# Kernel tuning notes

Measured on AMD Instinct MI355X. Metric: run time of the kernel, lower is better.

Reference implementation:

```python
import jax, jax.numpy as jnp
import numpy as np

B, P, J, MOT, K, NB, WN, H = 64, 12273, 80, 94, 64, 20, 17, 128
W_POSE = 1.0

def euler_to_rotmat(a):
    # a: [..., 3] radians, R = Rz @ Ry @ Rx
    sx, sy, sz = jnp.sin(a[..., 0]), jnp.sin(a[..., 1]), jnp.sin(a[..., 2])
    cx, cy, cz = jnp.cos(a[..., 0]), jnp.cos(a[..., 1]), jnp.cos(a[..., 2])
    r00 = cz * cy; r01 = cz * sy * sx - sz * cx; r02 = cz * sy * cx + sz * sx
    r10 = sz * cy; r11 = sz * sy * sx + cz * cx; r12 = sz * sy * cx - cz * sx
    r20 = -sy;     r21 = cy * sx;                r22 = cy * cx
    return jnp.stack([jnp.stack([r00, r01, r02], -1),
                      jnp.stack([r10, r11, r12], -1),
                      jnp.stack([r20, r21, r22], -1)], -2)

def setup_inputs() -> dict:
    key = jax.random.key(0)
    ks = jax.random.split(key, 20)
    f32 = jnp.float32
    return {
        'in_pc_batch': jax.random.normal(ks[0], (B, P, 3), f32),
        't_nor': jax.random.normal(ks[1], (B, P, 3), f32),
        'rest_verts': jax.random.normal(ks[2], (P, 3), f32),
        'skin_weights': jax.random.uniform(ks[3], (P, J), f32),
        'mul_weight_list': jax.random.normal(ks[4], (J, MOT), f32),
        'query': jax.random.normal(ks[5], (B, J, 3), f32),
        'cloth_pose_std': jax.random.uniform(ks[6], (3,), f32),
        'cloth_pose_mean': jax.random.normal(ks[7], (3,), f32),
        'cloth_trans_std': jax.random.uniform(ks[8], (3,), f32),
        'cloth_trans_mean': jax.random.normal(ks[9], (3,), f32),
        'W1': jax.random.normal(ks[10], (3 + K, H), f32) * 0.1,
        'b1': jnp.zeros((H,), f32),
        'W2': jax.random.normal(ks[11], (H, 6), f32) * 0.1,
        'b2': jnp.zeros((6,), f32),
        'tmtemp': jax.random.normal(ks[12], (B, MOT, K), f32),
        'Wd': jax.random.normal(ks[13], (MOT * K, NB * WN), f32) * 0.02,
        'bd': jnp.zeros((NB * WN,), f32),
        'DPSD': jax.random.normal(ks[14], (NB, WN, P, 3), f32) * 0.1,
        'ssdr_res_std': jax.random.uniform(ks[15], (3,), f32),
        'ssdr_res_mean': jax.random.normal(ks[16], (3,), f32),
    }

def reference(in_pc_batch, t_nor, rest_verts, skin_weights, mul_weight_list,
              query, cloth_pose_std, cloth_pose_mean, cloth_trans_std,
              cloth_trans_mean, W1, b1, W2, b2, tmtemp, Wd, bd, DPSD,
              ssdr_res_std, ssdr_res_mean):
    # per-joint field input: [B, J, K]
    field_input = jnp.einsum('bjk,lj->blk', tmtemp, jax.nn.relu(mul_weight_list))
    # FieldNet: per-joint MLP on concat(query, field_input) -> [B, J, 6]
    h = jnp.concatenate([query, field_input], axis=-1)
    pred_rt = jax.nn.relu(h @ W1 + b1) @ W2 + b2
    pred_pose = pred_rt[..., 0:3] * cloth_pose_std + cloth_pose_mean
    pred_trans = (query + pred_rt[..., 3:6]) * cloth_trans_std + cloth_trans_mean
    # detailsnet + fused 20-basis accumulation: [B, P, 3]
    nbat = tmtemp.shape[0]
    detailkey = (tmtemp.reshape(nbat, -1) @ Wd + bd).reshape(nbat, NB, WN)
    detail_res = jnp.einsum('bnw,nwpx->bpx', detailkey, DPSD)
    detail_res = detail_res * ssdr_res_std + ssdr_res_mean
    # SSDR LBS skinning with Euler-angle rotations (degrees -> radians)
    R = euler_to_rotmat(jnp.deg2rad(pred_pose))            # [B, J, 3, 3]
    skinned = (jnp.einsum('pj,bjxy,py->bpx', skin_weights, R, rest_verts)
               + jnp.einsum('pj,bjx->bpx', skin_weights, pred_trans))
    out_pc = skinned + detail_res                          # [B, P, 3]
    loss_pose_l1 = jnp.mean(jnp.abs(in_pc_batch[:, :, 0:3] - out_pc))
    loss = loss_pose_l1 * W_POSE + 1e-4 * jnp.mean(DPSD ** 2)
    return loss[None], out_pc
```

## Files before the change

kernel.cpp:

```cpp
#include <hip/hip_runtime.h>

#define B_   64
#define P_   12273
#define J_   80
#define MOT_ 94
#define K_   64
#define H_   128
#define Q_   340
#define NE_  36819
#define MK_  6016
#define PW_  12288
#define STG_ 2356416

typedef float v4f  __attribute__((ext_vector_type(4)));
typedef float v8f  __attribute__((ext_vector_type(8)));
typedef float v16f __attribute__((ext_vector_type(16)));
#define AS4 __attribute__((address_space(4)))

__device__ __forceinline__ const AS4 float* unif(const float* p){
  return (const AS4 float*)(unsigned long long)p;
}
__device__ __forceinline__ const AS4 v4f* univ4(const float* p){
  return (const AS4 v4f*)(unsigned long long)p;
}
__device__ __forceinline__ const AS4 v16f* univ16(const float* p){
  return (const AS4 v16f*)(unsigned long long)p;
}

__global__ __launch_bounds__(256) void k_prep(
    const float* __restrict__ query, const float* __restrict__ mwl,
    const float* __restrict__ tm,    const float* __restrict__ W1,
    const float* __restrict__ b1,    const float* __restrict__ W2,
    const float* __restrict__ b2,    const float* __restrict__ cps,
    const float* __restrict__ cpm,   const float* __restrict__ cts,
    const float* __restrict__ ctm,   const float* __restrict__ skin,
    float* __restrict__ G,           float* __restrict__ tm_t,
    float* __restrict__ w_t,         float* __restrict__ lacc)
{
  __shared__ float smem[80 * 65];
  int blk = blockIdx.x;
  int t = threadIdx.x;
  if (blk < 1280){
    int lane = t & 63;
    int wid = __builtin_amdgcn_readfirstlane(t >> 6);
    int bj = blk * 4 + wid;
    int b = bj / J_, l = bj - b * J_;
    float* hs = smem + wid * 80;
    float acc = 0.f;
    const AS4 float* mp = unif(mwl + l * MOT_);
    const float* tp = tm + (size_t)b * MK_ + lane;
    float tbuf[4];
    #pragma unroll
    for (int s = 0; s < 4; s++) tbuf[s] = tp[s * K_];
    #pragma unroll 4
    for (int j = 0; j < MOT_; j++){
      float tv = tbuf[j & 3];
      if (j + 4 < MOT_) tbuf[j & 3] = tp[(j + 4) * K_];
      float w = mp[j]; w = w > 0.f ? w : 0.f;
      acc = fmaf(w, tv, acc);
    }
    hs[3 + lane] = acc;
    if (lane < 3) hs[lane] = query[(size_t)bj * 3 + lane];
    __syncthreads();
    float a1 = b1[lane], a2 = b1[lane + 64];
    float wa[4], wb[4];
    #pragma unroll
    for (int s = 0; s < 4; s++){
      wa[s] = W1[s * H_ + lane];
      wb[s] = W1[s * H_ + 64 + lane];
    }
    #pragma unroll 4
    for (int i = 0; i < 67; i++){
      float hv = hs[i];
      float va = wa[i & 3], vb = wb[i & 3];
      if (i + 4 < 67){
        wa[i & 3] = W1[(i + 4) * H_ + lane];
        wb[i & 3] = W1[(i + 4) * H_ + 64 + lane];
      }
      a1 = fmaf(hv, va, a1);
      a2 = fmaf(hv, vb, a2);
    }
    a1 = a1 > 0.f ? a1 : 0.f;
    a2 = a2 > 0.f ? a2 : 0.f;
    const AS4 float* b2c = unif(b2);
    float rt[6];
    #pragma unroll
    for (int o = 0; o < 6; o++){
      float po = fmaf(a1, W2[lane * 6 + o], a2 * W2[(lane + 64) * 6 + o]);
      #pragma unroll
      for (int off = 32; off; off >>= 1) po += __shfl_xor(po, off);
      rt[o] = po + b2c[o];
    }
    const float D2R = 0.017453292519943295f;
    float ax = fmaf(rt[0], cps[0], cpm[0]) * D2R;
    float ay = fmaf(rt[1], cps[1], cpm[1]) * D2R;
    float az = fmaf(rt[2], cps[2], cpm[2]) * D2R;
    float tx = fmaf(hs[0] + rt[3], cts[0], ctm[0]);
    float ty = fmaf(hs[1] + rt[4], cts[1], ctm[1]);
    float tz = fmaf(hs[2] + rt[5], cts[2], ctm[2]);
    float sx, cx, sy, cy, sz, cz;
    sincosf(ax, &sx, &cx); sincosf(ay, &sy, &cy); sincosf(az, &sz, &cz);
    if (lane == 0){
      float4 r0 = make_float4(cz*cy, cz*sy*sx - sz*cx, cz*sy*cx + sz*sx, tx);
      float4 r1 = make_float4(sz*cy, sz*sy*sx + cz*cx, sz*sy*cx - cz*sx, ty);
      float4 r2 = make_float4(-sy,   cy*sx,            cy*cx,            tz);
      float4* g = (float4*)(G + (size_t)bj * 12);
      g[0] = r0; g[1] = r1; g[2] = r2;
    }
  } else if (blk < 1374){
    int m0 = (blk - 1280) * 64;
    int ml = t & 63, g = t >> 6;
    #pragma unroll
    for (int r = 0; r < 16; r++){
      int b = g * 16 + r;
      smem[ml * 65 + b] = tm[(size_t)b * MK_ + m0 + ml];
    }
    __syncthreads();
    int bl = t & 63;
    #pragma unroll
    for (int r = 0; r < 16; r++){
      int m = g * 16 + r;
      tm_t[(size_t)(m0 + m) * 64 + bl] = smem[m * 65 + bl];
    }
  } else if (blk < 1566){
    int p0 = (blk - 1374) * 64;
    #pragma unroll
    for (int k = 0; k < 20; k++){
      int idx = k * 256 + t;
      int pl = idx / 80, j = idx - pl * 80;
      int p = p0 + pl;
      smem[j * 65 + pl] = (p < P_) ? skin[(size_t)p * J_ + j] : 0.f;
    }
    __syncthreads();
    #pragma unroll
    for (int k = 0; k < 20; k++){
      int idx = k * 256 + t;
      int j = idx >> 6, pl = idx & 63;
      w_t[(size_t)j * PW_ + p0 + pl] = smem[j * 65 + pl];
    }
  } else {
    if (t < 2) lacc[t] = 0.f;
  }
}

__global__ __launch_bounds__(256) void k_dkey(
    const float* __restrict__ tm_t, const float* __restrict__ Wd,
    float* __restrict__ part)
{
  int t = threadIdx.x;
  int lane = t & 63;
  int wid = __builtin_amdgcn_readfirstlane(t >> 6);
  int qt = blockIdx.x;
  int q = qt * 64 + lane;
  bool vq = q < Q_;
  int m0 = blockIdx.y * 64;
  const AS4 v16f* tr = univ16(tm_t);
  float acc[16];
  #pragma unroll
  for (int i = 0; i < 16; i++) acc[i] = 0.f;
  float wbuf[4];
  #pragma unroll
  for (int i = 0; i < 4; i++)
    wbuf[i] = vq ? Wd[(size_t)(m0 + i) * Q_ + q] : 0.f;
  v16f tb0 = tr[(size_t)(m0 + 0) * 4 + wid];
  v16f tb1 = tr[(size_t)(m0 + 1) * 4 + wid];
  #pragma unroll 4
  for (int mm = 0; mm < 60; mm++){
    float wd = wbuf[mm & 3];
    wbuf[mm & 3] = vq ? Wd[(size_t)(m0 + mm + 4) * Q_ + q] : 0.f;
    v16f tv = tb0; tb0 = tb1;
    tb1 = tr[(size_t)(m0 + mm + 2) * 4 + wid];
    #pragma unroll
    for (int i = 0; i < 16; i++) acc[i] = fmaf(tv[i], wd, acc[i]);
  }
  #pragma unroll
  for (int mm = 60; mm < 64; mm++){
    float wd = wbuf[mm & 3];
    v16f tv = tb0; tb0 = tb1;
    if (mm < 62) tb1 = tr[(size_t)(m0 + mm + 2) * 4 + wid];
    #pragma unroll
    for (int i = 0; i < 16; i++) acc[i] = fmaf(tv[i], wd, acc[i]);
  }
  float* pb = part + ((size_t)blockIdx.y * 6 + qt) * 4096 + (size_t)(wid * 16) * 64;
  #pragma unroll
  for (int i = 0; i < 16; i++) pb[i * 64 + lane] = acc[i];
}

__global__ __launch_bounds__(256) void k_dkred(
    const float* __restrict__ part, const float* __restrict__ bd,
    float* __restrict__ dk_t, int S)
{
  int t = threadIdx.x;
  int jj = blockIdx.x * 32 + (t >> 3);
  int dl = t & 7;
  int b = jj / Q_, q = jj - b * Q_;
  int qt = q >> 6, ql = q & 63;
  const float* pp = part + (size_t)qt * 4096 + b * 64 + ql;
  float s = 0.f;
  for (int d = dl; d < S; d += 8) s += pp[(size_t)d * 6 * 4096];
  s += __shfl_xor(s, 1); s += __shfl_xor(s, 2); s += __shfl_xor(s, 4);
  if (dl == 0) dk_t[q * 64 + b] = bd[q] + s;
}

__device__ __forceinline__ void dk_consume(const AS4 v16f* dkv, int qa, int wid,
                                           const float* dc, float* acc,
                                           float& sq, bool doSq)
{
  v16f r0 = dkv[(qa + 0) * 4 + wid];
  v16f r1 = dkv[(qa + 1) * 4 + wid];
  v16f r2 = dkv[(qa + 2) * 4 + wid];
  v16f r3 = dkv[(qa + 3) * 4 + wid];
  v16f r4 = dkv[(qa + 4) * 4 + wid];
  if (doSq){
    #pragma unroll
    for (int i = 0; i < 5; i++) sq = fmaf(dc[i], dc[i], sq);
  }
  #pragma unroll
  for (int i = 0; i < 16; i++){
    acc[i] = fmaf(r0[i], dc[0], acc[i]);
    acc[i] = fmaf(r1[i], dc[1], acc[i]);
    acc[i] = fmaf(r2[i], dc[2], acc[i]);
    acc[i] = fmaf(r3[i], dc[3], acc[i]);
    acc[i] = fmaf(r4[i], dc[4], acc[i]);
  }
}

__global__ __launch_bounds__(256) void k_detail(
    const float* __restrict__ DPSD, const float* __restrict__ dk_t,
    float* __restrict__ stg, float* __restrict__ out,
    float* __restrict__ lacc, int qn)
{
  int t = threadIdx.x;
  int lane = t & 63;
  int wid = __builtin_amdgcn_readfirstlane(t >> 6);
  int b0 = wid * 16;
  int e = blockIdx.x * 64 + lane;
  bool ve = e < NE_;
  int q0 = blockIdx.y * qn;
  const AS4 v16f* dkv = univ16(dk_t);
  const float* Dp = DPSD + (ve ? e : 0);
  float acc[16];
  #pragma unroll
  for (int i = 0; i < 16; i++) acc[i] = 0.f;
  float sq = 0.f;
  bool doSq = (wid == 0);
  int ng = qn / 5;
  float buf[4][5];
  #pragma unroll
  for (int s = 0; s < 4; s++){
    #pragma unroll
    for (int i = 0; i < 5; i++)
      buf[s][i] = Dp[(size_t)(q0 + s * 5 + i) * NE_];
  }
  for (int g = 0; g < ng; g += 4){
    #pragma unroll
    for (int s = 0; s < 4; s++){
      int gg = g + s;
      if (gg < ng){
        dk_consume(dkv, q0 + gg * 5, wid, buf[s], acc, sq, doSq);
        int gp = gg + 4;
        if (gp < ng){
          #pragma unroll
          for (int i = 0; i < 5; i++)
            buf[s][i] = Dp[(size_t)(q0 + gp * 5 + i) * NE_];
        }
      }
    }
  }
  if (ve){
    bool toOut = (blockIdx.y + 1 == gridDim.y);
    float* dst = toOut ? (out + 1 + e) : (stg + (size_t)blockIdx.y * STG_ + e);
    #pragma unroll
    for (int i = 0; i < 16; i++)
      dst[(size_t)(b0 + i) * NE_] = acc[i];
  }
  if (doSq){
    if (!ve) sq = 0.f;
    #pragma unroll
    for (int off = 32; off; off >>= 1) sq += __shfl_xor(sq, off);
    if (lane == 0) atomicAdd(&lacc[1], sq);
  }
}

__global__ __launch_bounds__(256) void k_skin(
    const float* __restrict__ G, const float* __restrict__ w_t,
    const float* __restrict__ rest, const float* __restrict__ in_pc,
    const float* __restrict__ stg, const float* __restrict__ rstd,
    const float* __restrict__ rmean,
    float* __restrict__ out, float* __restrict__ lacc, int nst)
{
  __shared__ float gs[7680];
  __shared__ float red[4];
  int t = threadIdx.x;
  int lane = t & 63;
  int wid = __builtin_amdgcn_readfirstlane(t >> 6);
  {
    const float4* Gv = (const float4*)(G + (size_t)blockIdx.y * 7680);
    float4* gv = (float4*)gs;
    #pragma unroll
    for (int it = 0; it < 8; it++){
      int idx = it * 256 + t;
      if (idx < 1920) gv[idx] = Gv[idx];
    }
  }
  __syncthreads();
  int p  = blockIdx.x * 64 + lane;
  int bA = blockIdx.y * 8 + wid * 2;
  const float4* gsA = (const float4*)(gs + (wid * 2) * 960);
  const float4* gsB = gsA + 240;
  float accA[12], accB[12];
  #pragma unroll
  for (int c = 0; c < 12; c++){ accA[c] = 0.f; accB[c] = 0.f; }
  const float* wp = w_t + p;
  float wbuf[8];
  #pragma unroll
  for (int s = 0; s < 8; s++) wbuf[s] = wp[(size_t)s * PW_];
  #pragma unroll 8
  for (int j = 0; j < J_; j++){
    float w = wbuf[j & 7];
    if (j + 8 < J_) wbuf[j & 7] = wp[(size_t)(j + 8) * PW_];
    float4 a0 = gsA[j * 3], a1 = gsA[j * 3 + 1], a2 = gsA[j * 3 + 2];
    float4 c0 = gsB[j * 3], c1 = gsB[j * 3 + 1], c2 = gsB[j * 3 + 2];
    accA[0]  = fmaf(w, a0.x, accA[0]);  accA[1]  = fmaf(w, a0.y, accA[1]);
    accA[2]  = fmaf(w, a0.z, accA[2]);  accA[3]  = fmaf(w, a0.w, accA[3]);
    accA[4]  = fmaf(w, a1.x, accA[4]);  accA[5]  = fmaf(w, a1.y, accA[5]);
    accA[6]  = fmaf(w, a1.z, accA[6]);  accA[7]  = fmaf(w, a1.w, accA[7]);
    accA[8]  = fmaf(w, a2.x, accA[8]);  accA[9]  = fmaf(w, a2.y, accA[9]);
    accA[10] = fmaf(w, a2.z, accA[10]); accA[11] = fmaf(w, a2.w, accA[11]);
    accB[0]  = fmaf(w, c0.x, accB[0]);  accB[1]  = fmaf(w, c0.y, accB[1]);
    accB[2]  = fmaf(w, c0.z, accB[2]);  accB[3]  = fmaf(w, c0.w, accB[3]);
    accB[4]  = fmaf(w, c1.x, accB[4]);  accB[5]  = fmaf(w, c1.y, accB[5]);
    accB[6]  = fmaf(w, c1.z, accB[6]);  accB[7]  = fmaf(w, c1.w, accB[7]);
    accB[8]  = fmaf(w, c2.x, accB[8]);  accB[9]  = fmaf(w, c2.y, accB[9]);
    accB[10] = fmaf(w, c2.z, accB[10]); accB[11] = fmaf(w, c2.w, accB[11]);
  }
  bool vp = p < P_;
  float vx = 0.f, vy = 0.f, vz = 0.f;
  if (vp){ vx = rest[p * 3]; vy = rest[p * 3 + 1]; vz = rest[p * 3 + 2]; }
  float srs[3], srm[3];
  #pragma unroll
  for (int x = 0; x < 3; x++){ srs[x] = rstd[x]; srm[x] = rmean[x]; }
  float lsum = 0.f;
  if (vp){
    size_t baseA = ((size_t)bA * P_ + p) * 3;
    size_t baseB = baseA + (size_t)P_ * 3;
    #pragma unroll
    for (int x = 0; x < 3; x++){
      float det = out[1 + baseA + x];
      for (int s = 0; s < nst; s++) det += stg[(size_t)s * STG_ + baseA + x];
      float v = fmaf(accA[x*4+0], vx, fmaf(accA[x*4+1], vy, fmaf(accA[x*4+2], vz, accA[x*4+3])));
      v += fmaf(det, srs[x], srm[x]);
      lsum += fabsf(in_pc[baseA + x] - v);
      out[1 + baseA + x] = v;
    }
    #pragma unroll
    for (int x = 0; x < 3; x++){
      float det = out[1 + baseB + x];
      for (int s = 0; s < nst; s++) det += stg[(size_t)s * STG_ + baseB + x];
      float v = fmaf(accB[x*4+0], vx, fmaf(accB[x*4+1], vy, fmaf(accB[x*4+2], vz, accB[x*4+3])));
      v += fmaf(det, srs[x], srm[x]);
      lsum += fabsf(in_pc[baseB + x] - v);
      out[1 + baseB + x] = v;
    }
  }
  #pragma unroll
  for (int off = 32; off; off >>= 1) lsum += __shfl_xor(lsum, off);
  if (lane == 0) red[wid] = lsum;
  __syncthreads();
  if (t == 0) atomicAdd(&lacc[0], red[0] + red[1] + red[2] + red[3]);
}

__global__ void k_finalize(const float* __restrict__ lacc, float* __restrict__ out){
  if (threadIdx.x == 0 && blockIdx.x == 0){
    float loss = lacc[0] * (1.f / 2356416.f) + 1e-4f * (lacc[1] * (1.f / 12518460.f));
    out[0] = loss;
  }
}

extern "C" void kernel_launch(void* const* d_in, const int* in_sizes, int n_in,
                              void* d_out, int out_size, void* d_ws, size_t ws_size,
                              hipStream_t stream){
  const float* in_pc = (const float*)d_in[0];
  const float* rest  = (const float*)d_in[2];
  const float* skin  = (const float*)d_in[3];
  const float* mwl   = (const float*)d_in[4];
  const float* query = (const float*)d_in[5];
  const float* cps   = (const float*)d_in[6];
  const float* cpm   = (const float*)d_in[7];
  const float* cts   = (const float*)d_in[8];
  const float* ctm   = (const float*)d_in[9];
  const float* W1    = (const float*)d_in[10];
  const float* b1    = (const float*)d_in[11];
  const float* W2    = (const float*)d_in[12];
  const float* b2    = (const float*)d_in[13];
  const float* tm    = (const float*)d_in[14];
  const float* Wd    = (const float*)d_in[15];
  const float* bd    = (const float*)d_in[16];
  const float* DPSD  = (const float*)d_in[17];
  const float* rstd  = (const float*)d_in[18];
  const float* rmean = (const float*)d_in[19];
  float* out = (float*)d_out;

  float* ws   = (float*)d_ws;
  float* G    = ws;
  float* dk_t = G + 61440;
  float* lacc = dk_t + 21760;
  float* tm_t = lacc + 64;
  float* w_t  = tm_t + 385024;
  float* un   = w_t + 983040;

  size_t have = ws_size / 4;
  int nqh = (have >= (size_t)(1451328 + 2356416)) ? 2 : 1;
  int qn = Q_ / nqh;

  k_prep    <<<1567, 256, 0, stream>>>(query, mwl, tm, W1, b1, W2, b2,
                                       cps, cpm, cts, ctm, skin,
                                       G, tm_t, w_t, lacc);
  k_dkey    <<<dim3(6, 94), 256, 0, stream>>>(tm_t, Wd, un);
  k_dkred   <<<680, 256, 0, stream>>>(un, bd, dk_t, 94);
  k_detail  <<<dim3(576, nqh), 256, 0, stream>>>(DPSD, dk_t, un, out, lacc, qn);
  k_skin    <<<dim3(192, 8), 256, 0, stream>>>(G, w_t, rest, in_pc, un, rstd, rmean,
                                               out, lacc, nqh - 1);
  k_finalize<<<1, 64, 0, stream>>>(lacc, out);
}
```

Measured before the change: 310.3 us.

## Process two element columns per thread in detail and skin kernels

k_detail now has each thread handle two DPSD columns (e1, e2), so every detail-key vector loaded from constant memory feeds twice as many FMAs. The grid is halved and the software pipeline is restructured into a two-group double buffer. k_skin likewise processes two points per thread, drops the LDS staging of G in favour of scalar/constant loads, and halves its grid. This doubles register pressure and reduces occupancy and block count, which may expose memory latency in these bandwidth-heavy kernels.

Result: faster. 296.9 us (-4.3%).

```diff
diff --git a/kernel.cpp b/kernel.cpp
--- a/kernel.cpp
+++ b/kernel.cpp
@@ -202,26 +202,23 @@
   if (dl == 0) dk_t[q * 64 + b] = bd[q] + s;
 }
 
-__device__ __forceinline__ void dk_consume(const AS4 v16f* dkv, int qa, int wid,
-                                           const float* dc, float* acc,
-                                           float& sq, bool doSq)
-{
-  v16f r0 = dkv[(qa + 0) * 4 + wid];
-  v16f r1 = dkv[(qa + 1) * 4 + wid];
-  v16f r2 = dkv[(qa + 2) * 4 + wid];
-  v16f r3 = dkv[(qa + 3) * 4 + wid];
-  v16f r4 = dkv[(qa + 4) * 4 + wid];
-  if (doSq){
-    #pragma unroll
-    for (int i = 0; i < 5; i++) sq = fmaf(dc[i], dc[i], sq);
-  }
-  #pragma unroll
-  for (int i = 0; i < 16; i++){
-    acc[i] = fmaf(r0[i], dc[0], acc[i]);
-    acc[i] = fmaf(r1[i], dc[1], acc[i]);
-    acc[i] = fmaf(r2[i], dc[2], acc[i]);
-    acc[i] = fmaf(r3[i], dc[3], acc[i]);
-    acc[i] = fmaf(r4[i], dc[4], acc[i]);
+__device__ __forceinline__ void dk_consume2(const AS4 v16f* dkv, int qa, int wid,
+                                            const float* dc1, const float* dc2,
+                                            float* acc1, float* acc2,
+                                            float& sq1, float& sq2, bool doSq)
+{
+  #pragma unroll
+  for (int qi = 0; qi < 5; qi++){
+    v16f r = dkv[(size_t)(qa + qi) * 4 + wid];
+    if (doSq){
+      sq1 = fmaf(dc1[qi], dc1[qi], sq1);
+      sq2 = fmaf(dc2[qi], dc2[qi], sq2);
+    }
+    #pragma unroll
+    for (int i = 0; i < 16; i++){
+      acc1[i] = fmaf(r[i], dc1[qi], acc1[i]);
+      acc2[i] = fmaf(r[i], dc2[qi], acc2[i]);
+    }
   }
 }
 
@@ -234,48 +231,71 @@
   int lane = t & 63;
   int wid = __builtin_amdgcn_readfirstlane(t >> 6);
   int b0 = wid * 16;
-  int e = blockIdx.x * 64 + lane;
-  bool ve = e < NE_;
+  int e1 = blockIdx.x * 128 + lane;
+  int e2 = e1 + 64;
+  bool ve1 = e1 < NE_;
+  bool ve2 = e2 < NE_;
   int q0 = blockIdx.y * qn;
   const AS4 v16f* dkv = univ16(dk_t);
-  const float* Dp = DPSD + (ve ? e : 0);
-  float acc[16];
-  #pragma unroll
-  for (int i = 0; i < 16; i++) acc[i] = 0.f;
-  float sq = 0.f;
+  const float* Dp1 = DPSD + (ve1 ? e1 : 0);
+  const float* Dp2 = DPSD + (ve2 ? e2 : 0);
+  float acc1[16], acc2[16];
+  #pragma unroll
+  for (int i = 0; i < 16; i++){ acc1[i] = 0.f; acc2[i] = 0.f; }
+  float sq1 = 0.f, sq2 = 0.f;
   bool doSq = (wid == 0);
   int ng = qn / 5;
-  float buf[4][5];
-  #pragma unroll
-  for (int s = 0; s < 4; s++){
-    #pragma unroll
-    for (int i = 0; i < 5; i++)
-      buf[s][i] = Dp[(size_t)(q0 + s * 5 + i) * NE_];
-  }
-  for (int g = 0; g < ng; g += 4){
-    #pragma unroll
-    for (int s = 0; s < 4; s++){
-      int gg = g + s;
-      if (gg < ng){
-        dk_consume(dkv, q0 + gg * 5, wid, buf[s], acc, sq, doSq);
-        int gp = gg + 4;
-        if (gp < ng){
-          #pragma unroll
-          for (int i = 0; i < 5; i++)
-            buf[s][i] = Dp[(size_t)(q0 + gp * 5 + i) * NE_];
-        }
-      }
-    }
-  }
-  if (ve){
-    bool toOut = (blockIdx.y + 1 == gridDim.y);
-    float* dst = toOut ? (out + 1 + e) : (stg + (size_t)blockIdx.y * STG_ + e);
-    #pragma unroll
-    for (int i = 0; i < 16; i++)
-      dst[(size_t)(b0 + i) * NE_] = acc[i];
+  float da1[5], da2[5], db1[5], db2[5];
+  #pragma unroll
+  for (int i = 0; i < 5; i++){
+    da1[i] = Dp1[(size_t)(q0 + i) * NE_];
+    da2[i] = Dp2[(size_t)(q0 + i) * NE_];
+  }
+  #pragma unroll
+  for (int i = 0; i < 5; i++){
+    db1[i] = Dp1[(size_t)(q0 + 5 + i) * NE_];
+    db2[i] = Dp2[(size_t)(q0 + 5 + i) * NE_];
+  }
+  for (int g = 0; g + 2 < ng; g += 2){
+    int qa = q0 + g * 5;
+    float ta1[5], ta2[5], tb1[5], tb2[5];
+    #pragma unroll
+    for (int i = 0; i < 5; i++){
+      ta1[i] = Dp1[(size_t)(qa + 10 + i) * NE_];
+      ta2[i] = Dp2[(size_t)(qa + 10 + i) * NE_];
+    }
+    #pragma unroll
+    for (int i = 0; i < 5; i++){
+      tb1[i] = Dp1[(size_t)(qa + 15 + i) * NE_];
+      tb2[i] = Dp2[(size_t)(qa + 15 + i) * NE_];
+    }
+    dk_consume2(dkv, qa,     wid, da1, da2, acc1, acc2, sq1, sq2, doSq);
+    dk_consume2(dkv, qa + 5, wid, db1, db2, acc1, acc2, sq1, sq2, doSq);
+    #pragma unroll
+    for (int i = 0; i < 5; i++){ da1[i] = ta1[i]; da2[i] = ta2[i]; }
+    #pragma unroll
+    for (int i = 0; i < 5; i++){ db1[i] = tb1[i]; db2[i] = tb2[i]; }
+  }
+  dk_consume2(dkv, q0 + (ng - 2) * 5, wid, da1, da2, acc1, acc2, sq1, sq2, doSq);
+  dk_consume2(dkv, q0 + (ng - 1) * 5, wid, db1, db2, acc1, acc2, sq1, sq2, doSq);
+  bool toOut = (blockIdx.y + 1 == gridDim.y);
+  {
+    float* dst = (toOut ? (out + 1) : (stg + (size_t)blockIdx.y * STG_));
+    if (ve1){
+      #pragma unroll
+      for (int i = 0; i < 16; i++)
+        dst[(size_t)(b0 + i) * NE_ + e1] = acc1[i];
+    }
+    if (ve2){
+      #pragma unroll
+      for (int i = 0; i < 16; i++)
+        dst[(size_t)(b0 + i) * NE_ + e2] = acc2[i];
+    }
   }
   if (doSq){
-    if (!ve) sq = 0.f;
+    if (!ve1) sq1 = 0.f;
+    if (!ve2) sq2 = 0.f;
+    float sq = sq1 + sq2;
     #pragma unroll
     for (int off = 32; off; off >>= 1) sq += __shfl_xor(sq, off);
     if (lane == 0) atomicAdd(&lacc[1], sq);
@@ -289,66 +309,56 @@
     const float* __restrict__ rmean,
     float* __restrict__ out, float* __restrict__ lacc, int nst)
 {
-  __shared__ float gs[7680];
-  __shared__ float red[4];
   int t = threadIdx.x;
   int lane = t & 63;
   int wid = __builtin_amdgcn_readfirstlane(t >> 6);
-  {
-    const float4* Gv = (const float4*)(G + (size_t)blockIdx.y * 7680);
-    float4* gv = (float4*)gs;
-    #pragma unroll
-    for (int it = 0; it < 8; it++){
-      int idx = it * 256 + t;
-      if (idx < 1920) gv[idx] = Gv[idx];
-    }
-  }
-  __syncthreads();
-  int p  = blockIdx.x * 64 + lane;
+  int p1 = blockIdx.x * 128 + lane;
+  int p2 = p1 + 64;
   int bA = blockIdx.y * 8 + wid * 2;
-  const float4* gsA = (const float4*)(gs + (wid * 2) * 960);
-  const float4* gsB = gsA + 240;
-  float accA[12], accB[12];
-  #pragma unroll
-  for (int c = 0; c < 12; c++){ accA[c] = 0.f; accB[c] = 0.f; }
-  const float* wp = w_t + p;
-  float wbuf[8];
-  #pragma unroll
-  for (int s = 0; s < 8; s++) wbuf[s] = wp[(size_t)s * PW_];
-  #pragma unroll 8
+  const AS4 v4f* gA = univ4(G + (size_t)bA * J_ * 12);
+  const AS4 v4f* gB = univ4(G + ((size_t)bA + 1) * J_ * 12);
+  float aA1[12], aA2[12], aB1[12], aB2[12];
+  #pragma unroll
+  for (int c = 0; c < 12; c++){ aA1[c] = 0.f; aA2[c] = 0.f; aB1[c] = 0.f; aB2[c] = 0.f; }
+  const float* wp1 = w_t + p1;
+  const float* wp2 = w_t + p2;
+  #pragma unroll 2
   for (int j = 0; j < J_; j++){
-    float w = wbuf[j & 7];
-    if (j + 8 < J_) wbuf[j & 7] = wp[(size_t)(j + 8) * PW_];
-    float4 a0 = gsA[j * 3], a1 = gsA[j * 3 + 1], a2 = gsA[j * 3 + 2];
-    float4 c0 = gsB[j * 3], c1 = gsB[j * 3 + 1], c2 = gsB[j * 3 + 2];
-    accA[0]  = fmaf(w, a0.x, accA[0]);  accA[1]  = fmaf(w, a0.y, accA[1]);
-    accA[2]  = fmaf(w, a0.z, accA[2]);  accA[3]  = fmaf(w, a0.w, accA[3]);
-    accA[4]  = fmaf(w, a1.x, accA[4]);  accA[5]  = fmaf(w, a1.y, accA[5]);
-    accA[6]  = fmaf(w, a1.z, accA[6]);  accA[7]  = fmaf(w, a1.w, accA[7]);
-    accA[8]  = fmaf(w, a2.x, accA[8]);  accA[9]  = fmaf(w, a2.y, accA[9]);
-    accA[10] = fmaf(w, a2.z, accA[10]); accA[11] = fmaf(w, a2.w, accA[11]);
-    accB[0]  = fmaf(w, c0.x, accB[0]);  accB[1]  = fmaf(w, c0.y, accB[1]);
-    accB[2]  = fmaf(w, c0.z, accB[2]);  accB[3]  = fmaf(w, c0.w, accB[3]);
-    accB[4]  = fmaf(w, c1.x, accB[4]);  accB[5]  = fmaf(w, c1.y, accB[5]);
-    accB[6]  = fmaf(w, c1.z, accB[6]);  accB[7]  = fmaf(w, c1.w, accB[7]);
-    accB[8]  = fmaf(w, c2.x, accB[8]);  accB[9]  = fmaf(w, c2.y, accB[9]);
-    accB[10] = fmaf(w, c2.z, accB[10]); accB[11] = fmaf(w, c2.w, accB[11]);
-  }
-  bool vp = p < P_;
-  float vx = 0.f, vy = 0.f, vz = 0.f;
-  if (vp){ vx = rest[p * 3]; vy = rest[p * 3 + 1]; vz = rest[p * 3 + 2]; }
+    float w1 = wp1[(size_t)j * PW_];
+    float w2 = wp2[(size_t)j * PW_];
+    v4f a0 = gA[j * 3 + 0], a1 = gA[j * 3 + 1], a2 = gA[j * 3 + 2];
+    v4f c0 = gB[j * 3 + 0], c1 = gB[j * 3 + 1], c2 = gB[j * 3 + 2];
+    #pragma unroll
+    for (int c = 0; c < 4; c++){
+      aA1[c]     = fmaf(w1, a0[c], aA1[c]);
+      aA1[4 + c] = fmaf(w1, a1[c], aA1[4 + c]);
+      aA1[8 + c] = fmaf(w1, a2[c], aA1[8 + c]);
+      aA2[c]     = fmaf(w2, a0[c], aA2[c]);
+      aA2[4 + c] = fmaf(w2, a1[c], aA2[4 + c]);
+      aA2[8 + c] = fmaf(w2, a2[c], aA2[8 + c]);
+      aB1[c]     = fmaf(w1, c0[c], aB1[c]);
+      aB1[4 + c] = fmaf(w1, c1[c], aB1[4 + c]);
+      aB1[8 + c] = fmaf(w1, c2[c], aB1[8 + c]);
+      aB2[c]     = fmaf(w2, c0[c], aB2[c]);
+      aB2[4 + c] = fmaf(w2, c1[c], aB2[4 + c]);
+      aB2[8 + c] = fmaf(w2, c2[c], aB2[8 + c]);
+    }
+  }
   float srs[3], srm[3];
   #pragma unroll
   for (int x = 0; x < 3; x++){ srs[x] = rstd[x]; srm[x] = rmean[x]; }
   float lsum = 0.f;
-  if (vp){
-    size_t baseA = ((size_t)bA * P_ + p) * 3;
+  bool vp1 = p1 < P_;
+  bool vp2 = p2 < P_;
+  if (vp1){
+    float vx = rest[p1 * 3], vy = rest[p1 * 3 + 1], vz = rest[p1 * 3 + 2];
+    size_t baseA = ((size_t)bA * P_ + p1) * 3;
     size_t baseB = baseA + (size_t)P_ * 3;
     #pragma unroll
     for (int x = 0; x < 3; x++){
       float det = out[1 + baseA + x];
       for (int s = 0; s < nst; s++) det += stg[(size_t)s * STG_ + baseA + x];
-      float v = fmaf(accA[x*4+0], vx, fmaf(accA[x*4+1], vy, fmaf(accA[x*4+2], vz, accA[x*4+3])));
+      float v = fmaf(aA1[x*4+0], vx, fmaf(aA1[x*4+1], vy, fmaf(aA1[x*4+2], vz, aA1[x*4+3])));
       v += fmaf(det, srs[x], srm[x]);
       lsum += fabsf(in_pc[baseA + x] - v);
       out[1 + baseA + x] = v;
@@ -357,14 +367,38 @@
     for (int x = 0; x < 3; x++){
       float det = out[1 + baseB + x];
       for (int s = 0; s < nst; s++) det += stg[(size_t)s * STG_ + baseB + x];
-      float v = fmaf(accB[x*4+0], vx, fmaf(accB[x*4+1], vy, fmaf(accB[x*4+2], vz, accB[x*4+3])));
+      float v = fmaf(aB1[x*4+0], vx, fmaf(aB1[x*4+1], vy, fmaf(aB1[x*4+2], vz, aB1[x*4+3])));
       v += fmaf(det, srs[x], srm[x]);
       lsum += fabsf(in_pc[baseB + x] - v);
       out[1 + baseB + x] = v;
     }
   }
+  if (vp2){
+    float vx = rest[p2 * 3], vy = rest[p2 * 3 + 1], vz = rest[p2 * 3 + 2];
+    size_t baseA = ((size_t)bA * P_ + p2) * 3;
+    size_t baseB = baseA + (size_t)P_ * 3;
+    #pragma unroll
+    for (int x = 0; x < 3; x++){
+      float det = out[1 + baseA + x];
+      for (int s = 0; s < nst; s++) det += stg[(size_t)s * STG_ + baseA + x];
+      float v = fmaf(aA2[x*4+0], vx, fmaf(aA2[x*4+1], vy, fmaf(aA2[x*4+2], vz, aA2[x*4+3])));
+      v += fmaf(det, srs[x], srm[x]);
+      lsum += fabsf(in_pc[baseA + x] - v);
+      out[1 + baseA + x] = v;
+    }
+    #pragma unroll
+    for (int x = 0; x < 3; x++){
+      float det = out[1 + baseB + x];
+      for (int s = 0; s < nst; s++) det += stg[(size_t)s * STG_ + baseB + x];
+      float v = fmaf(aB2[x*4+0], vx, fmaf(aB2[x*4+1], vy, fmaf(aB2[x*4+2], vz, aB2[x*4+3])));
+      v += fmaf(det, srs[x], srm[x]);
+      lsum += fabsf(in_pc[baseB + x] - v);
+      out[1 + baseB + x] = v;
+    }
+  }
   #pragma unroll
   for (int off = 32; off; off >>= 1) lsum += __shfl_xor(lsum, off);
+  __shared__ float red[4];
   if (lane == 0) red[wid] = lsum;
   __syncthreads();
   if (t == 0) atomicAdd(&lacc[0], red[0] + red[1] + red[2] + red[3]);
@@ -418,8 +452,8 @@
                                        G, tm_t, w_t, lacc);
   k_dkey    <<<dim3(6, 94), 256, 0, stream>>>(tm_t, Wd, un);
   k_dkred   <<<680, 256, 0, stream>>>(un, bd, dk_t, 94);
-  k_detail  <<<dim3(576, nqh), 256, 0, stream>>>(DPSD, dk_t, un, out, lacc, qn);
-  k_skin    <<<dim3(192, 8), 256, 0, stream>>>(G, w_t, rest, in_pc, un, rstd, rmean,
-                                               out, lacc, nqh - 1);
+  k_detail  <<<dim3(288, nqh), 256, 0, stream>>>(DPSD, dk_t, un, out, lacc, qn);
+  k_skin    <<<dim3(96, 8), 256, 0, stream>>>(G, w_t, rest, in_pc, un, rstd, rmean,
+                                              out, lacc, nqh - 1);
   k_finalize<<<1, 64, 0, stream>>>(lacc, out);
 }
```
